# Kernel optimization log

Hardware: AMD Instinct MI355X
Metric: run time of the kernel (lower is better)

## Reference

```python
import jax, jax.numpy as jnp
import numpy as np

N = 50000      # total nodes across batched graphs
E = 400000     # directed edges (before self-loops)
B = 256        # number of graphs / protein embeddings
F_IN = 78      # atom features (num_features_xd)
H1, F1 = 10, 78   # gcn1: heads=10, out=78 -> concat 780
F2 = 128       # gcn2 output_dim (heads=1)
EMB = 320      # PLM embed_dim
PLM = 128      # plm_layers[0]
BN_EPS = 1e-5


def setup_inputs() -> dict:
    key = jax.random.key(0)
    ks = jax.random.split(key, 30)
    g = lambda k, s, sc=0.05: (jax.random.normal(k, s, jnp.float32) * sc)
    inp = {
        'x': jax.random.normal(ks[0], (N, F_IN), jnp.float32),
        'edge_index': jax.random.randint(ks[1], (2, E), 0, N),
        # deterministic sorted assignment guarantees every graph id in [0,B) is populated
        'batch': (jnp.arange(N) * B) // N,
        'target_embedding': jax.random.normal(ks[2], (B, EMB), jnp.float32),
        # GATConv 1 (78 -> 78, heads=10, concat)
        'W1': g(ks[3], (F_IN, H1 * F1)), 'a1s': g(ks[4], (H1, F1)), 'a1d': g(ks[5], (H1, F1)), 'b1': g(ks[6], (H1 * F1,)),
        # GATConv 2 (780 -> 128, heads=1)
        'W2': g(ks[7], (H1 * F1, F2)), 'a2s': g(ks[8], (1, F2)), 'a2d': g(ks[9], (1, F2)), 'b2': g(ks[10], (F2,)),
        # fc_g1
        'Wg': g(ks[11], (F2, F2)), 'bg': g(ks[12], (F2,)),
        # PLM branch: Linear(320,128) + BatchNorm1d(128) in eval mode
        'Wxt': g(ks[13], (EMB, PLM)), 'bxt': g(ks[14], (PLM,)),
        'gamma': jnp.ones((PLM,), jnp.float32), 'beta': jnp.zeros((PLM,), jnp.float32),
        'rmean': g(ks[15], (PLM,)), 'rvar': jax.random.uniform(ks[16], (PLM,), jnp.float32, 0.5, 1.5),
        # head MLP
        'Wf1': g(ks[17], (F2 + PLM, 1024)), 'bf1': g(ks[18], (1024,)),
        'Wf2': g(ks[19], (1024, 256)), 'bf2': g(ks[20], (256,)),
        'Wo': g(ks[21], (256, 1)), 'bo': g(ks[22], (1,)),
    }
    return inp


def gat_conv(x, src, dst, W, a_s, a_d, b, n):
    """PyG-style GATConv (self-loops already included in src/dst)."""
    H, F = a_s.shape
    h = (x @ W).reshape(-1, H, F)                        # [n, H, F]
    e = jax.nn.leaky_relu((h * a_s).sum(-1)[src] + (h * a_d).sum(-1)[dst], 0.2)  # [e, H]
    m = jax.ops.segment_max(e, dst, num_segments=n)      # segment softmax over incoming edges
    p = jnp.exp(e - m[dst])
    denom = jax.ops.segment_sum(p, dst, num_segments=n)
    alpha = p / denom[dst]                               # [e, H]
    out = jax.ops.segment_sum(alpha[:, :, None] * h[src], dst, num_segments=n)  # [n, H, F]
    return out.reshape(-1, H * F) + b


def reference(x, edge_index, batch, target_embedding, W1, a1s, a1d, b1, W2, a2s, a2d, b2,
              Wg, bg, Wxt, bxt, gamma, beta, rmean, rvar, Wf1, bf1, Wf2, bf2, Wo, bo):
    n = x.shape[0]
    loop = jnp.arange(n)
    src = jnp.concatenate([edge_index[0], loop])   # add self-loops (GATConv default)
    dst = jnp.concatenate([edge_index[1], loop])
    h = jax.nn.elu(gat_conv(x, src, dst, W1, a1s, a1d, b1, n))      # [N, 780]
    h = jax.nn.relu(gat_conv(h, src, dst, W2, a2s, a2d, b2, n))     # [N, 128]
    g = jax.ops.segment_max(h, batch, num_segments=B)               # global max pool [B, 128]
    g = jax.nn.relu(g @ Wg + bg)
    xt = target_embedding @ Wxt + bxt
    xt = jax.nn.relu((xt - rmean) / jnp.sqrt(rvar + BN_EPS) * gamma + beta)  # BN eval
    xc = jnp.concatenate([g, xt], axis=1)                           # [B, 256]
    xc = jax.nn.relu(xc @ Wf1 + bf1)
    xc = jax.nn.relu(xc @ Wf2 + bf2)
    return xc @ Wo + bo                                             # [B, 1]
```

## Files before the change

kernel.cpp:

```cpp
#include <hip/hip_runtime.h>
#include <hip/hip_fp16.h>
#include <math.h>

static constexpr int F2 = 128, EMB = 320;

typedef _Float16 h8v __attribute__((ext_vector_type(8)));
typedef float f4v __attribute__((ext_vector_type(4)));

union F4H2 { float4 f; __half2 h[4]; };
union F2H2 { float2 f; __half2 h[2]; };

__device__ __forceinline__ __half2 shfl_xor_h2(__half2 v, int off) {
    union { __half2 h; float f; } u;
    u.h = v;
    u.f = __shfl_xor(u.f, off);
    return u.h;
}

__device__ __forceinline__ void esd(const int* src, const int* dst, int E, int e, int& s, int& d) {
    if (e < E) { s = src[e]; d = dst[e]; }
    else       { s = e - E; d = s; }
}

__global__ void k_count(const int* __restrict__ src, const int* __restrict__ dst, int E, int Etot,
                        int* __restrict__ cnt) {
    int e = blockIdx.x * 256 + threadIdx.x;
    if (e >= Etot) return;
    int s, d;
    esd(src, dst, E, e, s, d);
    atomicAdd(&cnt[d], 1);
}

__global__ void k_scan1(const int* __restrict__ in, int* __restrict__ out, int* __restrict__ bsum,
                        int n) {
    __shared__ int tmp[256];
    int t = threadIdx.x;
    int gid = blockIdx.x * 256 + t;
    int v = gid < n ? in[gid] : 0;
    tmp[t] = v;
    __syncthreads();
    for (int off = 1; off < 256; off <<= 1) {
        int u = (t >= off) ? tmp[t - off] : 0;
        __syncthreads();
        tmp[t] += u;
        __syncthreads();
    }
    if (gid < n) out[gid] = tmp[t] - v;
    if (t == 255) bsum[blockIdx.x] = tmp[255];
}

__global__ void k_scan2(int* __restrict__ bsum, int nb) {
    __shared__ int tmp[256];
    __shared__ int carry;
    int t = threadIdx.x;
    if (t == 0) carry = 0;
    __syncthreads();
    for (int base = 0; base < nb; base += 256) {
        int i = base + t;
        int v = (i < nb) ? bsum[i] : 0;
        tmp[t] = v;
        __syncthreads();
        for (int off = 1; off < 256; off <<= 1) {
            int u = (t >= off) ? tmp[t - off] : 0;
            __syncthreads();
            tmp[t] += u;
            __syncthreads();
        }
        if (i < nb) bsum[i] = tmp[t] - v + carry;
        __syncthreads();
        if (t == 0) carry += tmp[255];
        __syncthreads();
    }
}

__global__ void k_scan3(int* __restrict__ out, const int* __restrict__ bsum, int n, int Etot,
                        int* __restrict__ rp_last, int* __restrict__ cur) {
    int gid = blockIdx.x * 256 + threadIdx.x;
    if (gid < n) {
        int v = out[gid] + bsum[blockIdx.x];
        out[gid] = v;
        cur[gid] = v;
    }
    if (gid == 0) rp_last[0] = Etot;
}

__global__ void k_scatter(const int* __restrict__ src, const int* __restrict__ dst, int E, int Etot,
                          int* __restrict__ cur, int* __restrict__ csrc) {
    int e = blockIdx.x * 256 + threadIdx.x;
    if (e >= Etot) return;
    int s, d;
    esd(src, dst, E, e, s, d);
    int pos = atomicAdd(&cur[d], 1);
    csrc[pos] = s;
}

__global__ void k_prep_w(const float* __restrict__ W1, const float* __restrict__ a1s,
                         const float* __restrict__ a1d, const float* __restrict__ W2,
                         __half* __restrict__ W1T, float* __restrict__ wes,
                         float* __restrict__ wed, __half* __restrict__ W2T) {
    int idx = blockIdx.x * 256 + threadIdx.x;
    if (idx < 76800) {
        int h = idx / (80 * 96), r = idx % (80 * 96), c = r / 96, k = r % 96;
        float v = (c < 78 && k < 78) ? W1[(size_t)k * 780 + h * 78 + c] : 0.f;
        W1T[idx] = __float2half(v);
    } else if (idx < 77600) {
        int j = idx - 76800;
        int h = j / 80, k = j % 80;
        float s = 0.f, d = 0.f;
        if (k < 78) {
            for (int f = 0; f < 78; f++) {
                float w = W1[(size_t)k * 780 + h * 78 + f];
                s = fmaf(w, a1s[h * 78 + f], s);
                d = fmaf(w, a1d[h * 78 + f], d);
            }
        }
        wes[j] = s;
        wed[j] = d;
    } else if (idx < 77600 + 128 * 800) {
        int j = idx - 77600;
        int c = j / 800, k = j % 800;
        float v = (k < 780) ? W2[(size_t)k * 128 + c] : 0.f;
        W2T[j] = __float2half(v);
    }
}

__global__ void k_prep_xpk(const float* __restrict__ x, __half2* __restrict__ xpk, int N) {
    int idx = blockIdx.x * 256 + threadIdx.x;
    if (idx >= N * 64) return;
    int n = idx >> 6, l = idx & 63;
    float lo = x[(size_t)n * 78 + l];
    float hi = (64 + l < 78) ? x[(size_t)n * 78 + 64 + l] : 0.f;
    xpk[idx] = __floats2half2_rn(lo, hi);
}

__global__ void k_coefx(const float* __restrict__ x, const float* __restrict__ wes,
                        const float* __restrict__ wed, float* __restrict__ esg,
                        float* __restrict__ edg, int N) {
    int n = blockIdx.x * 256 + threadIdx.x;
    if (n >= N) return;
    float es[10] = {}, ed[10] = {};
    const float* xr = x + (size_t)n * 78;
    for (int k = 0; k < 78; k++) {
        float xv = xr[k];
#pragma unroll
        for (int h = 0; h < 10; h++) {
            es[h] = fmaf(xv, wes[h * 80 + k], es[h]);
            ed[h] = fmaf(xv, wed[h * 80 + k], ed[h]);
        }
    }
#pragma unroll
    for (int h = 0; h < 10; h++) {
        esg[(size_t)n * 16 + h] = es[h];
        edg[(size_t)n * 16 + h] = ed[h];
    }
}

__global__ void k_gatx10(const int* __restrict__ rp, const int* __restrict__ csrc,
                         const float* __restrict__ esg, const float* __restrict__ edg,
                         const __half2* __restrict__ xpk, __half* __restrict__ xagg, int N) {
    __shared__ __align__(16) __half2 pl[4][64][12];
    __shared__ __align__(16) int sl[4][64];
    int w = threadIdx.x >> 6, lane = threadIdx.x & 63;
    int node = blockIdx.x * 4 + w;
    if (node >= N) return;
    int beg = rp[node], end = rp[node + 1];
    int deg = end - beg;

    float edn[10];
    {
        const float* ep = edg + (size_t)node * 16;
        float4 a = *(const float4*)ep, b = *(const float4*)(ep + 4);
        float2 c = *(const float2*)(ep + 8);
        edn[0] = a.x; edn[1] = a.y; edn[2] = a.z; edn[3] = a.w;
        edn[4] = b.x; edn[5] = b.y; edn[6] = b.z; edn[7] = b.w;
        edn[8] = c.x; edn[9] = c.y;
    }

    __half2 acc[10];
#pragma unroll
    for (int h = 0; h < 10; h++) acc[h] = __floats2half2_rn(0.f, 0.f);

#define PASSC_BODY(LIMIT)                                                          \
    for (int i0 = 0; i0 < (LIMIT); i0 += 4) {                                      \
        int4 s4 = *(const int4*)&sl[w][i0];                                        \
        __half2 xr0 = xpk[(size_t)s4.x * 64 + lane];                               \
        __half2 xr1 = xpk[(size_t)s4.y * 64 + lane];                               \
        __half2 xr2 = xpk[(size_t)s4.z * 64 + lane];                               \
        __half2 xr3 = xpk[(size_t)s4.w * 64 + lane];                               \
        _Pragma("unroll")                                                          \
        for (int j = 0; j < 4; j++) {                                              \
            F4H2 qa, qb; F2H2 qc;                                                  \
            qa.f = *(const float4*)&pl[w][i0 + j][0];                              \
            qb.f = *(const float4*)&pl[w][i0 + j][4];                              \
            qc.f = *(const float2*)&pl[w][i0 + j][8];                              \
            __half2 xr = (j == 0) ? xr0 : (j == 1) ? xr1 : (j == 2) ? xr2 : xr3;   \
            acc[0] = __hfma2(qa.h[0], xr, acc[0]);                                 \
            acc[1] = __hfma2(qa.h[1], xr, acc[1]);                                 \
            acc[2] = __hfma2(qa.h[2], xr, acc[2]);                                 \
            acc[3] = __hfma2(qa.h[3], xr, acc[3]);                                 \
            acc[4] = __hfma2(qb.h[0], xr, acc[4]);                                 \
            acc[5] = __hfma2(qb.h[1], xr, acc[5]);                                 \
            acc[6] = __hfma2(qb.h[2], xr, acc[6]);                                 \
            acc[7] = __hfma2(qb.h[3], xr, acc[7]);                                 \
            acc[8] = __hfma2(qc.h[0], xr, acc[8]);                                 \
            acc[9] = __hfma2(qc.h[1], xr, acc[9]);                                 \
        }                                                                          \
    }

#define STASH(PVEC)                                                                \
    {                                                                              \
        F4H2 wa, wb; F2H2 wc;                                                      \
        _Pragma("unroll")                                                          \
        for (int h = 0; h < 4; h++) wa.h[h] = __float2half2_rn(PVEC[h]);           \
        _Pragma("unroll")                                                          \
        for (int h = 0; h < 4; h++) wb.h[h] = __float2half2_rn(PVEC[4 + h]);       \
        wc.h[0] = __float2half2_rn(PVEC[8]);                                       \
        wc.h[1] = __float2half2_rn(PVEC[9]);                                       \
        *(float4*)&pl[w][lane][0] = wa.f;                                          \
        *(float4*)&pl[w][lane][4] = wb.f;                                          \
        *(float2*)&pl[w][lane][8] = wc.f;                                          \
        sl[w][lane] = s;                                                           \
    }

    if (deg <= 64) {
        bool act = lane < deg;
        int s = act ? csrc[beg + lane] : 0;
        float p[10];
        if (act) {
            const float* sp = esg + (size_t)s * 16;
            float4 a = *(const float4*)sp, b = *(const float4*)(sp + 4);
            float2 c = *(const float2*)(sp + 8);
            float v[10];
            v[0] = a.x + edn[0]; v[1] = a.y + edn[1]; v[2] = a.z + edn[2]; v[3] = a.w + edn[3];
            v[4] = b.x + edn[4]; v[5] = b.y + edn[5]; v[6] = b.z + edn[6]; v[7] = b.w + edn[7];
            v[8] = c.x + edn[8]; v[9] = c.y + edn[9];
#pragma unroll
            for (int h = 0; h < 10; h++) {
                float vv = v[h] >= 0.f ? v[h] : 0.2f * v[h];
                p[h] = __expf(vv);
            }
        } else {
#pragma unroll
            for (int h = 0; h < 10; h++) p[h] = 0.f;
        }
        __half2 sh[5];
#pragma unroll
        for (int j = 0; j < 5; j++) sh[j] = __floats2half2_rn(p[2 * j], p[2 * j + 1]);
        int start = (deg <= 16) ? 8 : 32;
        for (int off = start; off; off >>= 1) {
#pragma unroll
            for (int j = 0; j < 5; j++) sh[j] = __hadd2(sh[j], shfl_xor_h2(sh[j], off));
        }
#pragma unroll
        for (int j = 0; j < 5; j++) {
            float2 f = __half22float2(sh[j]);
            p[2 * j] *= 1.f / f.x;
            p[2 * j + 1] *= 1.f / f.y;
        }
        STASH(p)
        PASSC_BODY(deg)
    } else {
        float ssf[10] = {};
        for (int cb = beg; cb < end; cb += 64) {
            int e = cb + lane;
            bool act = e < end;
            int si = act ? csrc[e] : 0;
            if (act) {
                const float* sp = esg + (size_t)si * 16;
#pragma unroll
                for (int h = 0; h < 10; h++) {
                    float vv = sp[h] + edn[h];
                    vv = vv >= 0.f ? vv : 0.2f * vv;
                    ssf[h] += __expf(vv);
                }
            }
        }
#pragma unroll
        for (int off = 32; off; off >>= 1) {
#pragma unroll
            for (int h = 0; h < 10; h++) ssf[h] += __shfl_xor(ssf[h], off);
        }
        float inv[10];
#pragma unroll
        for (int h = 0; h < 10; h++) inv[h] = 1.f / ssf[h];

        for (int cb = beg; cb < end; cb += 64) {
            int cnt = min(64, end - cb);
            int e = cb + lane;
            bool act = e < end;
            int s = act ? csrc[e] : 0;
            float p[10];
            if (act) {
                const float* sp = esg + (size_t)s * 16;
#pragma unroll
                for (int h = 0; h < 10; h++) {
                    float vv = sp[h] + edn[h];
                    vv = vv >= 0.f ? vv : 0.2f * vv;
                    p[h] = __expf(vv) * inv[h];
                }
            } else {
#pragma unroll
                for (int h = 0; h < 10; h++) p[h] = 0.f;
            }
            STASH(p)
            PASSC_BODY(cnt)
        }
    }
#undef PASSC_BODY
#undef STASH

    __half* op = xagg + (size_t)node * 800;
#pragma unroll
    for (int h = 0; h < 10; h++) {
        __half* hp = op + h * 80;
        hp[lane] = __low2half(acc[h]);
        if (lane < 16) hp[64 + lane] = __high2half(acc[h]);
    }
}

__global__ __launch_bounds__(128) void k_gemmQ(const __half* __restrict__ xagg,
                                               const __half* __restrict__ W1T,
                                               const float* __restrict__ b1,
                                               const __half* __restrict__ W2T,
                                               const float* __restrict__ a2s,
                                               const float* __restrict__ a2d,
                                               __half* __restrict__ h216,
                                               float* __restrict__ es2,
                                               float* __restrict__ ed2, int N) {
    constexpr int LQ = 808;
    __shared__ __align__(16) _Float16 qlds[16 * LQ];
    __shared__ float sered[2][2][16];
    int w = threadIdx.x >> 6, lane = threadIdx.x & 63;
    int row0 = blockIdx.x * 16;
    int col16 = lane & 15, grp = lane >> 4;
    int ko = grp * 8;
    int rbase = grp * 4;
    int ar = min(row0 + col16, N - 1);

    for (int i = threadIdx.x; i < 16 * 28; i += 128) {
        int r = i / 28, c = 780 + i % 28;
        qlds[r * LQ + c] = (_Float16)0.f;
    }

    const _Float16* Ab = (const _Float16*)xagg + (size_t)ar * 800 + ko;
#pragma unroll
    for (int hh = 0; hh < 5; hh++) {
        int h = w * 5 + hh;
        f4v acc1[5] = {};
        const _Float16* Ap = Ab + h * 80;
        const _Float16* Bp = (const _Float16*)W1T + ((size_t)h * 80 + col16) * 96 + ko;
#pragma unroll
        for (int ks = 0; ks < 3; ks++) {
            h8v a = *(const h8v*)(Ap + ks * 32);
#pragma unroll
            for (int t = 0; t < 5; t++) {
                h8v b = *(const h8v*)(Bp + (size_t)t * 16 * 96 + ks * 32);
                acc1[t] = __builtin_amdgcn_mfma_f32_16x16x32_f16(a, b, acc1[t], 0, 0, 0);
            }
        }
#pragma unroll
        for (int t = 0; t < 5; t++) {
            int c = t * 16 + col16;
            if (c < 78) {
                float bias = b1[h * 78 + c];
#pragma unroll
                for (int r = 0; r < 4; r++) {
                    float v = acc1[t][r] + bias;
                    float e = v > 0.f ? v : (__expf(v) - 1.f);
                    qlds[(rbase + r) * LQ + h * 78 + c] = (_Float16)e;
                }
            }
        }
    }
    __syncthreads();

    f4v acc[4] = {};
    const _Float16* Bq = (const _Float16*)W2T + (size_t)col16 * 800 + ko;
    const _Float16* Aq = qlds + (size_t)col16 * LQ + ko;
    for (int ks = 0; ks < 25; ks++) {
        h8v a = *(const h8v*)(Aq + ks * 32);
#pragma unroll
        for (int t = 0; t < 4; t++) {
            h8v b = *(const h8v*)(Bq + (size_t)(w * 4 + t) * 16 * 800 + ks * 32);
            acc[t] = __builtin_amdgcn_mfma_f32_16x16x32_f16(a, b, acc[t], 0, 0, 0);
        }
    }
    float wa[4], wb[4];
#pragma unroll
    for (int t = 0; t < 4; t++) {
        wa[t] = a2s[(w * 4 + t) * 16 + col16];
        wb[t] = a2d[(w * 4 + t) * 16 + col16];
    }
#pragma unroll
    for (int r = 0; r < 4; r++) {
        int n = row0 + rbase + r;
        float se = 0.f, sd = 0.f;
#pragma unroll
        for (int t = 0; t < 4; t++) {
            float v = acc[t][r];
            se = fmaf(v, wa[t], se);
            sd = fmaf(v, wb[t], sd);
            if (n < N) h216[(size_t)n * 128 + (w * 4 + t) * 16 + col16] = __float2half(v);
        }
#pragma unroll
        for (int off = 1; off < 16; off <<= 1) {
            se += __shfl_xor(se, off);
            sd += __shfl_xor(sd, off);
        }
        if (col16 == 0) {
            sered[w][0][rbase + r] = se;
            sered[w][1][rbase + r] = sd;
        }
    }
    __syncthreads();
    if (threadIdx.x < 16) {
        int n = row0 + threadIdx.x;
        if (n < N) {
            es2[n] = sered[0][0][threadIdx.x] + sered[1][0][threadIdx.x];
            ed2[n] = sered[0][1][threadIdx.x] + sered[1][1][threadIdx.x];
        }
    }
}

__global__ void k_gatP(const int* __restrict__ rp, const int* __restrict__ csrc,
                       const float* __restrict__ es, const float* __restrict__ ed,
                       const __half2* __restrict__ h216, const float* __restrict__ b2,
                       const int* __restrict__ batch, unsigned* __restrict__ gb, int N) {
    __shared__ float red[4][128];
    __shared__ int bids[4];
    __shared__ __align__(16) __half2 plP[4][64];
    __shared__ __align__(16) int slP[4][64];
    int w = threadIdx.x >> 6, lane = threadIdx.x & 63;
    int node = blockIdx.x * 4 + w;
    bool valid = node < N;

    __half2 acc = __floats2half2_rn(0.f, 0.f);
    int bid = -1;

#define PASSC2(LIMIT)                                                      \
    for (int i0 = 0; i0 < (LIMIT); i0 += 4) {                              \
        int4 s4 = *(const int4*)&slP[w][i0];                               \
        F4H2 q; q.f = *(const float4*)&plP[w][i0];                         \
        __half2 f0 = h216[(size_t)s4.x * 64 + lane];                       \
        __half2 f1 = h216[(size_t)s4.y * 64 + lane];                       \
        __half2 f2 = h216[(size_t)s4.z * 64 + lane];                       \
        __half2 f3 = h216[(size_t)s4.w * 64 + lane];                       \
        acc = __hfma2(q.h[0], f0, acc);                                    \
        acc = __hfma2(q.h[1], f1, acc);                                    \
        acc = __hfma2(q.h[2], f2, acc);                                    \
        acc = __hfma2(q.h[3], f3, acc);                                    \
    }

    if (valid) {
        int beg = rp[node], end = rp[node + 1];
        int deg = end - beg;
        float edn = ed[node];
        bid = batch[node];

        if (deg <= 64) {
            bool act = lane < deg;
            int s = act ? csrc[beg + lane] : 0;
            float p = 0.f;
            if (act) {
                float v = es[s] + edn;
                v = v >= 0.f ? v : 0.2f * v;
                p = __expf(v);
            }
            float ss = p;
            int start = (deg <= 16) ? 8 : 32;
            for (int off = start; off; off >>= 1) ss += __shfl_xor(ss, off);
            p *= 1.f / ss;
            plP[w][lane] = __float2half2_rn(p);
            slP[w][lane] = s;
            PASSC2(deg)
        } else {
            float ss = 0.f;
            for (int cb = beg; cb < end; cb += 64) {
                int e = cb + lane;
                bool act = e < end;
                int s = act ? csrc[e] : 0;
                if (act) {
                    float v = es[s] + edn;
                    v = v >= 0.f ? v : 0.2f * v;
                    ss += __expf(v);
                }
            }
#pragma unroll
            for (int off = 32; off; off >>= 1) ss += __shfl_xor(ss, off);
            float inv = 1.f / ss;
            for (int cb = beg; cb < end; cb += 64) {
                int cnt = min(64, end - cb);
                int e = cb + lane;
                bool act = e < end;
                int s = act ? csrc[e] : 0;
                float p = 0.f;
                if (act) {
                    float v = es[s] + edn;
                    v = v >= 0.f ? v : 0.2f * v;
                    p = __expf(v) * inv;
                }
                plP[w][lane] = __float2half2_rn(p);
                slP[w][lane] = s;
                PASSC2(cnt)
            }
        }
    }
#undef PASSC2

    float2 af = __half22float2(acc);
    red[w][2 * lane]     = valid ? fmaxf(af.x + b2[2 * lane], 0.f) : 0.f;
    red[w][2 * lane + 1] = valid ? fmaxf(af.y + b2[2 * lane + 1], 0.f) : 0.f;
    if (lane == 0) bids[w] = valid ? bid : -1;
    __syncthreads();
    if (threadIdx.x < 128) {
        int c = threadIdx.x;
        int b0 = bids[0];
        bool same = (bids[1] == b0) && (bids[2] == b0) && (bids[3] == b0);
        if (same && b0 >= 0) {
            float m = fmaxf(fmaxf(red[0][c], red[1][c]), fmaxf(red[2][c], red[3][c]));
            atomicMax(&gb[(size_t)b0 * 128 + c], __float_as_uint(m));
        } else {
#pragma unroll
            for (int w2 = 0; w2 < 4; w2++) {
                if (bids[w2] >= 0)
                    atomicMax(&gb[(size_t)bids[w2] * 128 + c], __float_as_uint(red[w2][c]));
            }
        }
    }
}

__global__ void k_head_gxt(const unsigned* __restrict__ gbits, const float* __restrict__ Wg,
                           const float* __restrict__ bg, const float* __restrict__ te,
                           const float* __restrict__ Wxt, const float* __restrict__ bxt,
                           const float* __restrict__ gamma, const float* __restrict__ beta,
                           const float* __restrict__ rmean, const float* __restrict__ rvar,
                           float* __restrict__ xc) {
    __shared__ float sg[F2];
    __shared__ float st[EMB];
    int b = blockIdx.x, t = threadIdx.x;
    if (t < 128) {
        sg[t] = __uint_as_float(gbits[(size_t)b * F2 + t]);
    } else {
        for (int k = t - 128; k < EMB; k += 128) st[k] = te[(size_t)b * EMB + k];
    }
    __syncthreads();
    if (t < 128) {
        float acc = bg[t];
        for (int k = 0; k < F2; k++) acc = fmaf(sg[k], Wg[k * F2 + t], acc);
        xc[(size_t)b * 256 + t] = fmaxf(acc, 0.f);
    } else {
        int c = t - 128;
        float acc = bxt[c];
        for (int k = 0; k < EMB; k++) acc = fmaf(st[k], Wxt[k * F2 + c], acc);
        acc = (acc - rmean[c]) * rsqrtf(rvar[c] + 1e-5f) * gamma[c] + beta[c];
        xc[(size_t)b * 256 + 128 + c] = fmaxf(acc, 0.f);
    }
}

__global__ void k_head_mlp(const float* __restrict__ xc, const float* __restrict__ Wf1,
                           const float* __restrict__ bf1, const float* __restrict__ Wf2,
                           const float* __restrict__ bf2, const float* __restrict__ Wo,
                           const float* __restrict__ bo, float* __restrict__ out) {
    __shared__ float s0[256];
    __shared__ float s1[1024];
    int b = blockIdx.x, t = threadIdx.x;
    s0[t] = xc[(size_t)b * 256 + t];
    __syncthreads();
    for (int col = t; col < 1024; col += 256) {
        float acc = bf1[col];
        for (int k = 0; k < 256; k++) acc = fmaf(s0[k], Wf1[k * 1024 + col], acc);
        s1[col] = fmaxf(acc, 0.f);
    }
    __syncthreads();
    {
        float acc = bf2[t];
        for (int k = 0; k < 1024; k++) acc = fmaf(s1[k], Wf2[k * 256 + t], acc);
        float v = fmaxf(acc, 0.f);
        __syncthreads();
        s0[t] = v * Wo[t];
    }
    __syncthreads();
    if (t < 64) {
        float acc = s0[t] + s0[64 + t] + s0[128 + t] + s0[192 + t];
        for (int off = 32; off; off >>= 1) acc += __shfl_down(acc, off);
        if (t == 0) out[b] = acc + bo[0];
    }
}

extern "C" void kernel_launch(void* const* d_in, const int* in_sizes, int n_in,
                              void* d_out, int out_size, void* d_ws, size_t ws_size,
                              hipStream_t stream) {
    const float* x     = (const float*)d_in[0];
    const int*   ei    = (const int*)d_in[1];
    const int*   batch = (const int*)d_in[2];
    const float* te    = (const float*)d_in[3];
    const float* W1    = (const float*)d_in[4];
    const float* a1s   = (const float*)d_in[5];
    const float* a1d   = (const float*)d_in[6];
    const float* b1    = (const float*)d_in[7];
    const float* W2    = (const float*)d_in[8];
    const float* a2s   = (const float*)d_in[9];
    const float* a2d   = (const float*)d_in[10];
    const float* b2    = (const float*)d_in[11];
    const float* Wg    = (const float*)d_in[12];
    const float* bg    = (const float*)d_in[13];
    const float* Wxt   = (const float*)d_in[14];
    const float* bxt   = (const float*)d_in[15];
    const float* gamma = (const float*)d_in[16];
    const float* beta  = (const float*)d_in[17];
    const float* rmean = (const float*)d_in[18];
    const float* rvar  = (const float*)d_in[19];
    const float* Wf1   = (const float*)d_in[20];
    const float* bf1   = (const float*)d_in[21];
    const float* Wf2   = (const float*)d_in[22];
    const float* bf2   = (const float*)d_in[23];
    const float* Wo    = (const float*)d_in[24];
    const float* bo    = (const float*)d_in[25];

    const int N = in_sizes[0] / 78;
    const int E = in_sizes[1] / 2;
    const int B = in_sizes[3] / EMB;
    const int Etot = E + N;
    const int* src = ei;
    const int* dst = ei + E;

    char* p = (char*)d_ws;
    auto alloc = [&](size_t bytes) -> void* {
        void* r = p;
        p += (bytes + 255) & ~(size_t)255;
        return r;
    };
    __half2*  xpk  = (__half2*)alloc((size_t)N * 64 * 4);
    __half*   xagg = (__half*)alloc((size_t)N * 800 * 2 + 256);
    __half*   h216 = (__half*)alloc((size_t)N * 128 * 2);
    float*    esg  = (float*)alloc((size_t)N * 16 * 4);
    float*    edg  = (float*)alloc((size_t)N * 16 * 4);
    float*    es2  = (float*)alloc((size_t)N * 4);
    float*    ed2  = (float*)alloc((size_t)N * 4);
    __half*   W1T  = (__half*)alloc((size_t)10 * 80 * 96 * 2);
    __half*   W2T  = (__half*)alloc((size_t)128 * 800 * 2);
    float*    wes  = (float*)alloc((size_t)800 * 4);
    float*    wed  = (float*)alloc((size_t)800 * 4);
    int*      cnt  = (int*)alloc((size_t)N * 4);
    int*      rp   = (int*)alloc((size_t)(N + 1) * 4);
    int*      cur  = (int*)alloc((size_t)N * 4);
    int*      csrc = (int*)alloc((size_t)Etot * 4);
    int*      bsum = (int*)alloc((size_t)1024 * 4);
    unsigned* gb   = (unsigned*)alloc((size_t)B * F2 * 4);
    float*    xc   = (float*)alloc((size_t)B * 256 * 4);

    auto gsz = [](long long t) { return (int)((t + 255) / 256); };
    const int nb = gsz(N);
    const int nwave = (N + 3) / 4;
    const int nrow16 = (N + 15) / 16;

    hipMemsetAsync(cnt, 0, (size_t)N * 4, stream);
    k_count<<<gsz(Etot), 256, 0, stream>>>(src, dst, E, Etot, cnt);
    k_scan1<<<nb, 256, 0, stream>>>(cnt, rp, bsum, N);
    k_scan2<<<1, 256, 0, stream>>>(bsum, nb);
    k_scan3<<<nb, 256, 0, stream>>>(rp, bsum, N, Etot, rp + N, cur);
    k_scatter<<<gsz(Etot), 256, 0, stream>>>(src, dst, E, Etot, cur, csrc);

    k_prep_w<<<gsz(77600 + 128 * 800), 256, 0, stream>>>(W1, a1s, a1d, W2, W1T, wes, wed, W2T);
    k_prep_xpk<<<gsz((long long)N * 64), 256, 0, stream>>>(x, xpk, N);
    k_coefx<<<nb, 256, 0, stream>>>(x, wes, wed, esg, edg, N);
    hipMemsetAsync(gb, 0, (size_t)B * F2 * 4, stream);

    k_gatx10<<<nwave, 256, 0, stream>>>(rp, csrc, esg, edg, xpk, xagg, N);

    k_gemmQ<<<nrow16, 128, 0, stream>>>(xagg, W1T, b1, W2T, a2s, a2d, h216, es2, ed2, N);

    k_gatP<<<nwave, 256, 0, stream>>>(rp, csrc, es2, ed2, (const __half2*)h216, b2, batch, gb, N);

    k_head_gxt<<<B, 256, 0, stream>>>(gb, Wg, bg, te, Wxt, bxt, gamma, beta, rmean, rvar, xc);
    k_head_mlp<<<B, 256, 0, stream>>>(xc, Wf1, bf1, Wf2, bf2, Wo, bo, (float*)d_out);
}
```

Before: 335.0 us.

## Retile fused GAT GEMM to 32-row blocks with 8 waves

The fused layer-1 output plus layer-2 projection kernel now processes 32 node rows per block with 512 threads instead of 16 rows with 128 threads. Each wave owns one 16-column slice of the 128 outputs and reuses each W2 fragment across two 16-row A tiles. The aim is to halve redundant W2 loads per row and raise parallelism per block. In exchange it needs twice the shared memory per block, adds an extra barrier for the reduction that reuses the LDS buffer, and launches fewer blocks.

```diff
diff --git a/kernel.cpp b/kernel.cpp
--- a/kernel.cpp
+++ b/kernel.cpp
@@ -318,7 +318,7 @@
     }
 }
 
-__global__ __launch_bounds__(128) void k_gemmQ(const __half* __restrict__ xagg,
+__global__ __launch_bounds__(512) void k_gemmQ(const __half* __restrict__ xagg,
                                                const __half* __restrict__ W1T,
                                                const float* __restrict__ b1,
                                                const __half* __restrict__ W2T,
@@ -328,27 +328,24 @@
                                                float* __restrict__ es2,
                                                float* __restrict__ ed2, int N) {
     constexpr int LQ = 808;
-    __shared__ __align__(16) _Float16 qlds[16 * LQ];
-    __shared__ float sered[2][2][16];
+    __shared__ __align__(16) _Float16 qlds[32 * LQ];
     int w = threadIdx.x >> 6, lane = threadIdx.x & 63;
-    int row0 = blockIdx.x * 16;
+    int row0 = blockIdx.x * 32;
     int col16 = lane & 15, grp = lane >> 4;
     int ko = grp * 8;
     int rbase = grp * 4;
-    int ar = min(row0 + col16, N - 1);
-
-    for (int i = threadIdx.x; i < 16 * 28; i += 128) {
+
+    for (int i = threadIdx.x; i < 32 * 28; i += 512) {
         int r = i / 28, c = 780 + i % 28;
         qlds[r * LQ + c] = (_Float16)0.f;
     }
 
-    const _Float16* Ab = (const _Float16*)xagg + (size_t)ar * 800 + ko;
-#pragma unroll
-    for (int hh = 0; hh < 5; hh++) {
-        int h = w * 5 + hh;
+    for (int j = w; j < 20; j += 8) {
+        int h = j >> 1, half = j & 1;
+        int ar = min(row0 + half * 16 + col16, N - 1);
+        const _Float16* Ap = (const _Float16*)xagg + (size_t)ar * 800 + h * 80 + ko;
+        const _Float16* Bp = (const _Float16*)W1T + ((size_t)h * 80 + col16) * 96 + ko;
         f4v acc1[5] = {};
-        const _Float16* Ap = Ab + h * 80;
-        const _Float16* Bp = (const _Float16*)W1T + ((size_t)h * 80 + col16) * 96 + ko;
 #pragma unroll
         for (int ks = 0; ks < 3; ks++) {
             h8v a = *(const h8v*)(Ap + ks * 32);
@@ -367,57 +364,68 @@
                 for (int r = 0; r < 4; r++) {
                     float v = acc1[t][r] + bias;
                     float e = v > 0.f ? v : (__expf(v) - 1.f);
-                    qlds[(rbase + r) * LQ + h * 78 + c] = (_Float16)e;
+                    qlds[(half * 16 + rbase + r) * LQ + h * 78 + c] = (_Float16)e;
                 }
             }
         }
     }
     __syncthreads();
 
-    f4v acc[4] = {};
-    const _Float16* Bq = (const _Float16*)W2T + (size_t)col16 * 800 + ko;
-    const _Float16* Aq = qlds + (size_t)col16 * LQ + ko;
+    f4v acc0 = {}, acc1 = {};
+    const _Float16* Bq = (const _Float16*)W2T + ((size_t)w * 16 + col16) * 800 + ko;
+    const _Float16* Aq0 = qlds + (size_t)col16 * LQ + ko;
+    const _Float16* Aq1 = qlds + (size_t)(16 + col16) * LQ + ko;
     for (int ks = 0; ks < 25; ks++) {
-        h8v a = *(const h8v*)(Aq + ks * 32);
-#pragma unroll
-        for (int t = 0; t < 4; t++) {
-            h8v b = *(const h8v*)(Bq + (size_t)(w * 4 + t) * 16 * 800 + ks * 32);
-            acc[t] = __builtin_amdgcn_mfma_f32_16x16x32_f16(a, b, acc[t], 0, 0, 0);
-        }
-    }
-    float wa[4], wb[4];
-#pragma unroll
-    for (int t = 0; t < 4; t++) {
-        wa[t] = a2s[(w * 4 + t) * 16 + col16];
-        wb[t] = a2d[(w * 4 + t) * 16 + col16];
-    }
-#pragma unroll
-    for (int r = 0; r < 4; r++) {
-        int n = row0 + rbase + r;
-        float se = 0.f, sd = 0.f;
-#pragma unroll
-        for (int t = 0; t < 4; t++) {
-            float v = acc[t][r];
-            se = fmaf(v, wa[t], se);
-            sd = fmaf(v, wb[t], sd);
-            if (n < N) h216[(size_t)n * 128 + (w * 4 + t) * 16 + col16] = __float2half(v);
-        }
-#pragma unroll
-        for (int off = 1; off < 16; off <<= 1) {
-            se += __shfl_xor(se, off);
-            sd += __shfl_xor(sd, off);
-        }
-        if (col16 == 0) {
-            sered[w][0][rbase + r] = se;
-            sered[w][1][rbase + r] = sd;
-        }
-    }
-    __syncthreads();
-    if (threadIdx.x < 16) {
+        h8v b = *(const h8v*)(Bq + ks * 32);
+        h8v a0 = *(const h8v*)(Aq0 + ks * 32);
+        h8v a1 = *(const h8v*)(Aq1 + ks * 32);
+        acc0 = __builtin_amdgcn_mfma_f32_16x16x32_f16(a0, b, acc0, 0, 0, 0);
+        acc1 = __builtin_amdgcn_mfma_f32_16x16x32_f16(a1, b, acc1, 0, 0, 0);
+    }
+    float wa = a2s[w * 16 + col16], wb = a2d[w * 16 + col16];
+    float sse[2][4], ssd[2][4];
+#pragma unroll
+    for (int rb = 0; rb < 2; rb++) {
+#pragma unroll
+        for (int r = 0; r < 4; r++) {
+            int n = row0 + rb * 16 + rbase + r;
+            float v = rb ? acc1[r] : acc0[r];
+            float se = v * wa, sd = v * wb;
+#pragma unroll
+            for (int off = 1; off < 16; off <<= 1) {
+                se += __shfl_xor(se, off);
+                sd += __shfl_xor(sd, off);
+            }
+            sse[rb][r] = se;
+            ssd[rb][r] = sd;
+            if (n < N) h216[(size_t)n * 128 + w * 16 + col16] = __float2half(v);
+        }
+    }
+    __syncthreads();
+    float* seredf = (float*)qlds;
+    if (col16 == 0) {
+#pragma unroll
+        for (int rb = 0; rb < 2; rb++) {
+#pragma unroll
+            for (int r = 0; r < 4; r++) {
+                int rowi = rb * 16 + rbase + r;
+                seredf[w * 64 + rowi] = sse[rb][r];
+                seredf[w * 64 + 32 + rowi] = ssd[rb][r];
+            }
+        }
+    }
+    __syncthreads();
+    if (threadIdx.x < 32) {
         int n = row0 + threadIdx.x;
         if (n < N) {
-            es2[n] = sered[0][0][threadIdx.x] + sered[1][0][threadIdx.x];
-            ed2[n] = sered[0][1][threadIdx.x] + sered[1][1][threadIdx.x];
+            float es = 0.f, ed = 0.f;
+#pragma unroll
+            for (int ww = 0; ww < 8; ww++) {
+                es += seredf[ww * 64 + threadIdx.x];
+                ed += seredf[ww * 64 + 32 + threadIdx.x];
+            }
+            es2[n] = es;
+            ed2[n] = ed;
         }
     }
 }
@@ -652,7 +660,7 @@
     auto gsz = [](long long t) { return (int)((t + 255) / 256); };
     const int nb = gsz(N);
     const int nwave = (N + 3) / 4;
-    const int nrow16 = (N + 15) / 16;
+    const int nrow32 = (N + 31) / 32;
 
     hipMemsetAsync(cnt, 0, (size_t)N * 4, stream);
     k_count<<<gsz(Etot), 256, 0, stream>>>(src, dst, E, Etot, cnt);
@@ -668,7 +676,7 @@
 
     k_gatx10<<<nwave, 256, 0, stream>>>(rp, csrc, esg, edg, xpk, xagg, N);
 
-    k_gemmQ<<<nrow16, 128, 0, stream>>>(xagg, W1T, b1, W2T, a2s, a2d, h216, es2, ed2, N);
+    k_gemmQ<<<nrow32, 512, 0, stream>>>(xagg, W1T, b1, W2T, a2s, a2d, h216, es2, ed2, N);
 
     k_gatP<<<nwave, 256, 0, stream>>>(rp, csrc, es2, ed2, (const __half2*)h216, b2, batch, gb, N);
 
```

After: 311.3 us. 1.08x faster.
